# Performance work log

Measured on AMD Instinct MI355X. Metric: run time of the kernel, lower is better.

## Reference

```python
import jax, jax.numpy as jnp
import numpy as np

INPUT_SIZE = 1024
HIDDEN_SIZE = 1024
BATCH = 8192


def setup_inputs() -> dict:
    key = jax.random.key(0)
    ks = jax.random.split(key, 10)
    s_in = 1.0 / np.sqrt(INPUT_SIZE)
    s_h = 1.0 / np.sqrt(HIDDEN_SIZE)
    return {
        "input": jax.random.normal(ks[0], (BATCH, INPUT_SIZE), jnp.float32),
        "hx": jax.random.normal(ks[1], (BATCH, HIDDEN_SIZE), jnp.float32),
        # weights stored [in, out] (transpose of torch Linear)
        "W_ih": jax.random.uniform(ks[2], (INPUT_SIZE, 2 * HIDDEN_SIZE), jnp.float32, -s_in, s_in),
        "b_ih": jax.random.uniform(ks[3], (2 * HIDDEN_SIZE,), jnp.float32, -s_in, s_in),
        "W_hh": jax.random.uniform(ks[4], (HIDDEN_SIZE, 2 * HIDDEN_SIZE), jnp.float32, -s_h, s_h),
        "b_hh": jax.random.uniform(ks[5], (2 * HIDDEN_SIZE,), jnp.float32, -s_h, s_h),
        "W_c": jax.random.uniform(ks[6], (INPUT_SIZE, HIDDEN_SIZE), jnp.float32, -s_in, s_in),
        "b_c": jax.random.uniform(ks[7], (HIDDEN_SIZE,), jnp.float32, -s_in, s_in),
        "W_hc": jax.random.uniform(ks[8], (HIDDEN_SIZE, HIDDEN_SIZE), jnp.float32, -s_h, s_h),
        "b_hc": jax.random.uniform(ks[9], (HIDDEN_SIZE,), jnp.float32, -s_h, s_h),
    }


def reference(input, hx, W_ih, b_ih, W_hh, b_hh, W_c, b_c, W_hc, b_hc):
    H = hx.shape[1]
    gates = jax.nn.sigmoid(input @ W_ih + b_ih + hx @ W_hh + b_hh)  # [B, 2H]
    z_t, r_t = gates[:, :H], gates[:, H:]
    candidate = jnp.tanh(input @ W_c + b_c + r_t * (hx @ W_hc + b_hc))
    return (1.0 - z_t) * hx + z_t * candidate
```

## Files before the change

kernel.cpp:

```cpp
#include <hip/hip_runtime.h>
#include <hip/hip_bf16.h>
#include <cmath>


typedef __attribute__((ext_vector_type(8))) short bf16x8;
typedef __attribute__((ext_vector_type(4))) float f32x4;
typedef unsigned int u32;

typedef const __attribute__((address_space(1))) u32 gu32;
typedef __attribute__((address_space(3))) u32 su32;

__device__ __forceinline__ unsigned short f2bf(float f) {
  union { float f; u32 u; } v; v.f = f;
  u32 u = v.u;
  u += 0x7FFFu + ((u >> 16) & 1u);
  return (unsigned short)(u >> 16);
}

__device__ __forceinline__ void gload16(void* ldsp, const void* gp) {
  __builtin_amdgcn_global_load_lds((gu32*)gp, (su32*)ldsp, 16, 0, 0);
}

__device__ __forceinline__ float sigmf(float x) { return 1.0f / (1.0f + __expf(-x)); }

__global__ __launch_bounds__(256) void cvt_all(
    const float* __restrict__ In, const float* __restrict__ Hx,
    const float* __restrict__ Wih, const float* __restrict__ Whh,
    const float* __restrict__ Wc,  const float* __restrict__ Whc,
    unsigned short* __restrict__ wsIn, unsigned short* __restrict__ wsHx,
    unsigned short* __restrict__ wsWih, unsigned short* __restrict__ wsWhh,
    unsigned short* __restrict__ wsWc,  unsigned short* __restrict__ wsWhc)
{
  int bid = blockIdx.x;
  if (bid < 8192) {
    int gid = bid * 256 + threadIdx.x;
    const float* src; unsigned short* dst; int idx;
    if (gid < (1 << 20)) { src = In; dst = wsIn; idx = gid; }
    else                 { src = Hx; dst = wsHx; idx = gid - (1 << 20); }
    int m = idx >> 7;
    int t = idx & 127;
    const float4* s = (const float4*)(src + (size_t)m * 1024 + t * 8);
    float4 a = s[0], b = s[1];
    int row = m & 127;
    size_t tile = (size_t)(m >> 7) * 32 + (t >> 2);
    int sw = (t & 3) ^ ((row >> 1) & 3);
    bf16x8 v;
    v[0] = (short)f2bf(a.x); v[1] = (short)f2bf(a.y); v[2] = (short)f2bf(a.z); v[3] = (short)f2bf(a.w);
    v[4] = (short)f2bf(b.x); v[5] = (short)f2bf(b.y); v[6] = (short)f2bf(b.z); v[7] = (short)f2bf(b.w);
    *(bf16x8*)(dst + tile * 4096 + row * 32 + sw * 8) = v;
  } else {
    int wb = bid - 8192;
    const float* W; unsigned short* dst; int NW; int local;
    if (wb < 1024)      { W = Wih; dst = wsWih; NW = 2048; local = wb; }
    else if (wb < 2048) { W = Whh; dst = wsWhh; NW = 2048; local = wb - 1024; }
    else if (wb < 2560) { W = Wc;  dst = wsWc;  NW = 1024; local = wb - 2048; }
    else                { W = Whc; dst = wsWhc; NW = 1024; local = wb - 2560; }
    int nb = local >> 5, kb = local & 31;
    int n  = nb * 64 + (threadIdx.x & 63);
    int k0 = kb * 32 + (threadIdx.x >> 6) * 8;
    unsigned short h[8];
    #pragma unroll
    for (int b = 0; b < 8; ++b) h[b] = f2bf(W[(size_t)(k0 + b) * NW + n]);
    int row = n & 63;
    size_t tile = (size_t)(n >> 6) * 32 + (k0 >> 5);
    int sw = ((k0 >> 3) & 3) ^ ((row >> 1) & 3);
    bf16x8 v;
    #pragma unroll
    for (int b = 0; b < 8; ++b) v[b] = (short)h[b];
    *(bf16x8*)(dst + tile * 2048 + row * 32 + sw * 8) = v;
  }
}

__global__ __launch_bounds__(512, 2) void gru_gemm(
    const unsigned short* __restrict__ wsIn, const unsigned short* __restrict__ wsHx,
    const unsigned short* __restrict__ wsWih, const unsigned short* __restrict__ wsWhh,
    const unsigned short* __restrict__ wsWc, const unsigned short* __restrict__ wsWhc,
    const float* __restrict__ Hx,
    const float* __restrict__ bih, const float* __restrict__ bhh,
    const float* __restrict__ bc, const float* __restrict__ bhc,
    float* __restrict__ out)
{
  __shared__ unsigned short lds[57344];
  const int tid  = threadIdx.x;
  const int lane = tid & 63;
  const int wave = tid >> 6;
  const int wm = wave >> 1, wn = wave & 1;
  const int bid = blockIdx.x;
  const int swz = (bid & 7) * 64 + (bid >> 3);
  const int j = swz & 15;
  const int i = swz >> 4;

  const unsigned short* srcB[7];
  int strd[7];
  #pragma unroll
  for (int c0 = 0; c0 < 7; ++c0) {
    int c = wave * 7 + c0;
    const unsigned short* p; int st;
    if (c < 16) {
      int mt = 2 * i + (c >> 3);
      p = wsIn + (size_t)mt * 131072 + (c & 7) * 512; st = 4096;
    } else if (c < 32) {
      int cc = c - 16; int mt = 2 * i + (cc >> 3);
      p = wsHx + (size_t)mt * 131072 + (cc & 7) * 512; st = 4096;
    } else {
      int t = (c - 32) >> 2, cc = (c - 32) & 3;
      const unsigned short* base; int nb;
      if (t == 0)      { base = wsWih; nb = j; }
      else if (t == 1) { base = wsWih; nb = j + 16; }
      else if (t == 2) { base = wsWhh; nb = j; }
      else if (t == 3) { base = wsWhh; nb = j + 16; }
      else if (t == 4) { base = wsWc;  nb = j; }
      else             { base = wsWhc; nb = j; }
      p = base + (size_t)nb * 65536 + cc * 512; st = 2048;
    }
    srcB[c0] = p + lane * 8;
    strd[c0] = st;
  }
  const int ldsC = wave * 3584;

  f32x4 accZ[4][2], accR[4][2], accC[4][2], accH[4][2];
  #pragma unroll
  for (int a = 0; a < 4; ++a)
    #pragma unroll
    for (int b = 0; b < 2; ++b) {
      accZ[a][b] = (f32x4)(0.0f); accR[a][b] = (f32x4)(0.0f);
      accC[a][b] = (f32x4)(0.0f); accH[a][b] = (f32x4)(0.0f);
    }

  const int r15 = lane & 15;
  const int q   = lane >> 4;

  int aOff[4], wOff[2];
  #pragma unroll
  for (int mr = 0; mr < 4; ++mr) {
    int gr = wm * 64 + mr * 16 + r15;
    aOff[mr] = (gr >> 7) * 4096 + (gr & 127) * 32 + ((q ^ ((gr >> 1) & 3)) << 3);
  }
  #pragma unroll
  for (int nr = 0; nr < 2; ++nr) {
    int wr = wn * 32 + nr * 16 + r15;
    wOff[nr] = 16384 + wr * 32 + ((q ^ ((wr >> 1) & 3)) << 3);
  }

  auto stage = [&](int B, int s) {
    #pragma unroll
    for (int c0 = 0; c0 < 7; ++c0)
      gload16((void*)&lds[B + ldsC + c0 * 512],
              (const void*)(srcB[c0] + (size_t)s * strd[c0]));
  };

  auto step = [&](int B, int s2) {
    bf16x8 aIn[4], aHx[4];
    #pragma unroll
    for (int mr = 0; mr < 4; ++mr) {
      aIn[mr] = *(const bf16x8*)&lds[B + aOff[mr]];
      aHx[mr] = *(const bf16x8*)&lds[B + 8192 + aOff[mr]];
    }
    __builtin_amdgcn_s_setprio(1);
    {
      bf16x8 wa[2], wb[2];
      #pragma unroll
      for (int nr = 0; nr < 2; ++nr) {
        wa[nr] = *(const bf16x8*)&lds[B + wOff[nr]];
        wb[nr] = *(const bf16x8*)&lds[B + 4096 + wOff[nr]];
      }
      #pragma unroll
      for (int mr = 0; mr < 4; ++mr)
        #pragma unroll
        for (int nr = 0; nr < 2; ++nr) {
          accZ[mr][nr] = __builtin_amdgcn_mfma_f32_16x16x32_bf16(aIn[mr], wa[nr], accZ[mr][nr], 0, 0, 0);
          accZ[mr][nr] = __builtin_amdgcn_mfma_f32_16x16x32_bf16(aHx[mr], wb[nr], accZ[mr][nr], 0, 0, 0);
        }
    }
    {
      bf16x8 wa[2], wb[2];
      #pragma unroll
      for (int nr = 0; nr < 2; ++nr) {
        wa[nr] = *(const bf16x8*)&lds[B + 2048 + wOff[nr]];
        wb[nr] = *(const bf16x8*)&lds[B + 6144 + wOff[nr]];
      }
      #pragma unroll
      for (int mr = 0; mr < 4; ++mr)
        #pragma unroll
        for (int nr = 0; nr < 2; ++nr) {
          accR[mr][nr] = __builtin_amdgcn_mfma_f32_16x16x32_bf16(aIn[mr], wa[nr], accR[mr][nr], 0, 0, 0);
          accR[mr][nr] = __builtin_amdgcn_mfma_f32_16x16x32_bf16(aHx[mr], wb[nr], accR[mr][nr], 0, 0, 0);
        }
    }
    {
      bf16x8 wa[2], wb[2];
      #pragma unroll
      for (int nr = 0; nr < 2; ++nr) {
        wa[nr] = *(const bf16x8*)&lds[B + 8192 + wOff[nr]];
        wb[nr] = *(const bf16x8*)&lds[B + 10240 + wOff[nr]];
      }
      #pragma unroll
      for (int mr = 0; mr < 4; ++mr)
        #pragma unroll
        for (int nr = 0; nr < 2; ++nr) {
          accC[mr][nr] = __builtin_amdgcn_mfma_f32_16x16x32_bf16(aIn[mr], wa[nr], accC[mr][nr], 0, 0, 0);
          accH[mr][nr] = __builtin_amdgcn_mfma_f32_16x16x32_bf16(aHx[mr], wb[nr], accH[mr][nr], 0, 0, 0);
        }
    }
    __builtin_amdgcn_s_setprio(0);
    asm volatile("s_waitcnt lgkmcnt(0)" ::: "memory");
    __builtin_amdgcn_s_barrier();
    stage(B, s2);
    asm volatile("s_waitcnt vmcnt(7)" ::: "memory");
    __builtin_amdgcn_s_barrier();
  };

  stage(0, 0);
  stage(28672, 1);
  asm volatile("s_waitcnt vmcnt(7)" ::: "memory");
  __builtin_amdgcn_s_barrier();

  #pragma unroll 1
  for (int it = 0; it < 16; ++it) {
    const int s = it * 2;
    step(0,     s + 2 <= 31 ? s + 2 : 31);
    step(28672, s + 3 <= 31 ? s + 3 : 31);
  }

  const int n0 = j * 64 + wn * 32;
  const int m0 = i * 256 + wm * 64;
  #pragma unroll
  for (int nr = 0; nr < 2; ++nr) {
    int n = n0 + nr * 16 + r15;
    float bz  = bih[n] + bhh[n];
    float br  = bih[1024 + n] + bhh[1024 + n];
    float bcv = bc[n], bhcv = bhc[n];
    #pragma unroll
    for (int mr = 0; mr < 4; ++mr) {
      #pragma unroll
      for (int v = 0; v < 4; ++v) {
        int m = m0 + mr * 16 + q * 4 + v;
        float z  = sigmf(accZ[mr][nr][v] + bz);
        float rr = sigmf(accR[mr][nr][v] + br);
        float cd = tanhf(accC[mr][nr][v] + bcv + rr * (accH[mr][nr][v] + bhcv));
        float h  = Hx[(size_t)m * 1024 + n];
        out[(size_t)m * 1024 + n] = (1.0f - z) * h + z * cd;
      }
    }
  }
}

__global__ __launch_bounds__(256) void gru_fallback(
    const float* __restrict__ In, const float* __restrict__ Hx,
    const float* __restrict__ Wih, const float* __restrict__ bih,
    const float* __restrict__ Whh, const float* __restrict__ bhh,
    const float* __restrict__ Wc, const float* __restrict__ bc,
    const float* __restrict__ Whc, const float* __restrict__ bhc,
    float* __restrict__ out)
{
  __shared__ float sIn[64][17], sHx[64][17];
  __shared__ float sW[6][16][68];
  const int tid = threadIdx.x;
  const int j = blockIdx.x & 15, i = blockIdx.x >> 4;
  const int tx = tid & 15, ty = tid >> 4;
  float accZ[4][4] = {}, accR[4][4] = {}, accC[4][4] = {}, accH[4][4] = {};
  const int ms = tid >> 2, kq = (tid & 3) * 4;
  const int wk = tid >> 4, wn4 = (tid & 15) * 4;
  for (int k0 = 0; k0 < 1024; k0 += 16) {
    __syncthreads();
    {
      float4 a = *(const float4*)&In[(size_t)(i * 64 + ms) * 1024 + k0 + kq];
      sIn[ms][kq] = a.x; sIn[ms][kq + 1] = a.y; sIn[ms][kq + 2] = a.z; sIn[ms][kq + 3] = a.w;
      float4 b = *(const float4*)&Hx[(size_t)(i * 64 + ms) * 1024 + k0 + kq];
      sHx[ms][kq] = b.x; sHx[ms][kq + 1] = b.y; sHx[ms][kq + 2] = b.z; sHx[ms][kq + 3] = b.w;
    }
    {
      float4 w0 = *(const float4*)&Wih[(size_t)(k0 + wk) * 2048 + j * 64 + wn4];
      float4 w1 = *(const float4*)&Wih[(size_t)(k0 + wk) * 2048 + 1024 + j * 64 + wn4];
      float4 w2 = *(const float4*)&Whh[(size_t)(k0 + wk) * 2048 + j * 64 + wn4];
      float4 w3 = *(const float4*)&Whh[(size_t)(k0 + wk) * 2048 + 1024 + j * 64 + wn4];
      float4 w4 = *(const float4*)&Wc[(size_t)(k0 + wk) * 1024 + j * 64 + wn4];
      float4 w5 = *(const float4*)&Whc[(size_t)(k0 + wk) * 1024 + j * 64 + wn4];
      sW[0][wk][wn4] = w0.x; sW[0][wk][wn4+1] = w0.y; sW[0][wk][wn4+2] = w0.z; sW[0][wk][wn4+3] = w0.w;
      sW[1][wk][wn4] = w1.x; sW[1][wk][wn4+1] = w1.y; sW[1][wk][wn4+2] = w1.z; sW[1][wk][wn4+3] = w1.w;
      sW[2][wk][wn4] = w2.x; sW[2][wk][wn4+1] = w2.y; sW[2][wk][wn4+2] = w2.z; sW[2][wk][wn4+3] = w2.w;
      sW[3][wk][wn4] = w3.x; sW[3][wk][wn4+1] = w3.y; sW[3][wk][wn4+2] = w3.z; sW[3][wk][wn4+3] = w3.w;
      sW[4][wk][wn4] = w4.x; sW[4][wk][wn4+1] = w4.y; sW[4][wk][wn4+2] = w4.z; sW[4][wk][wn4+3] = w4.w;
      sW[5][wk][wn4] = w5.x; sW[5][wk][wn4+1] = w5.y; sW[5][wk][wn4+2] = w5.z; sW[5][wk][wn4+3] = w5.w;
    }
    __syncthreads();
    for (int kk = 0; kk < 16; ++kk) {
      float aI[4], aH[4];
      #pragma unroll
      for (int im = 0; im < 4; ++im) { aI[im] = sIn[ty * 4 + im][kk]; aH[im] = sHx[ty * 4 + im][kk]; }
      #pragma unroll
      for (int jn = 0; jn < 4; ++jn) {
        float w0 = sW[0][kk][tx * 4 + jn], w1 = sW[1][kk][tx * 4 + jn], w2 = sW[2][kk][tx * 4 + jn];
        float w3 = sW[3][kk][tx * 4 + jn], w4 = sW[4][kk][tx * 4 + jn], w5 = sW[5][kk][tx * 4 + jn];
        #pragma unroll
        for (int im = 0; im < 4; ++im) {
          accZ[im][jn] += aI[im] * w0 + aH[im] * w2;
          accR[im][jn] += aI[im] * w1 + aH[im] * w3;
          accC[im][jn] += aI[im] * w4;
          accH[im][jn] += aH[im] * w5;
        }
      }
    }
  }
  #pragma unroll
  for (int jn = 0; jn < 4; ++jn) {
    int n = j * 64 + tx * 4 + jn;
    float bz  = bih[n] + bhh[n];
    float br  = bih[1024 + n] + bhh[1024 + n];
    float bcv = bc[n], bhcv = bhc[n];
    #pragma unroll
    for (int im = 0; im < 4; ++im) {
      int m = i * 64 + ty * 4 + im;
      float z  = sigmf(accZ[im][jn] + bz);
      float rr = sigmf(accR[im][jn] + br);
      float cd = tanhf(accC[im][jn] + bcv + rr * (accH[im][jn] + bhcv));
      float h  = Hx[(size_t)m * 1024 + n];
      out[(size_t)m * 1024 + n] = (1.0f - z) * h + z * cd;
    }
  }
}

extern "C" void kernel_launch(void* const* d_in, const int* in_sizes, int n_in,
                              void* d_out, int out_size, void* d_ws, size_t ws_size,
                              hipStream_t stream) {
  const float* In  = (const float*)d_in[0];
  const float* Hx  = (const float*)d_in[1];
  const float* Wih = (const float*)d_in[2];
  const float* bih = (const float*)d_in[3];
  const float* Whh = (const float*)d_in[4];
  const float* bhh = (const float*)d_in[5];
  const float* Wc  = (const float*)d_in[6];
  const float* bc  = (const float*)d_in[7];
  const float* Whc = (const float*)d_in[8];
  const float* bhc = (const float*)d_in[9];
  float* out = (float*)d_out;

  const size_t WS_NEED = 46137344ull;
  if (ws_size >= WS_NEED) {
    unsigned short* ws    = (unsigned short*)d_ws;
    unsigned short* wsIn  = ws;
    unsigned short* wsHx  = ws + 8388608;
    unsigned short* wsWih = ws + 16777216;
    unsigned short* wsWhh = ws + 18874368;
    unsigned short* wsWc  = ws + 20971520;
    unsigned short* wsWhc = ws + 22020096;
    cvt_all<<<11264, 256, 0, stream>>>(In, Hx, Wih, Whh, Wc, Whc,
                                       wsIn, wsHx, wsWih, wsWhh, wsWc, wsWhc);
    gru_gemm<<<512, 512, 0, stream>>>(wsIn, wsHx, wsWih, wsWhh, wsWc, wsWhc,
                                      Hx, bih, bhh, bc, bhc, out);
  } else {
    gru_fallback<<<2048, 256, 0, stream>>>(In, Hx, Wih, bih, Whh, bhh, Wc, bc, Whc, bhc, out);
  }
}
```

Before: 135.6 us.

## Interleave global-to-LDS staging between MFMA phases within each k-step

Restructures the main GEMM loop so the next-stage global_load_lds copies are issued piecewise between the Z, R and C/H MFMA phases instead of all after compute. The LDS layout is reordered so the weight chunks consumed first are loaded earliest, with one chunk (Wc/Whc) prefetched into the other buffer a step ahead. The aim is to overlap memory traffic with tensor-core work, at the cost of more barriers per step and a more fragile wait-count scheme.

```diff
diff --git a/kernel.cpp b/kernel.cpp
--- a/kernel.cpp
+++ b/kernel.cpp
@@ -16,12 +16,14 @@
   u += 0x7FFFu + ((u >> 16) & 1u);
   return (unsigned short)(u >> 16);
 }
-
 __device__ __forceinline__ void gload16(void* ldsp, const void* gp) {
   __builtin_amdgcn_global_load_lds((gu32*)gp, (su32*)ldsp, 16, 0, 0);
 }
-
 __device__ __forceinline__ float sigmf(float x) { return 1.0f / (1.0f + __expf(-x)); }
+
+#define LGKM0 do { asm volatile("s_waitcnt lgkmcnt(0)" ::: "memory"); __builtin_amdgcn_sched_barrier(0); } while (0)
+#define VMC6  do { asm volatile("s_waitcnt vmcnt(6)"   ::: "memory"); __builtin_amdgcn_sched_barrier(0); } while (0)
+#define BARR  __builtin_amdgcn_s_barrier()
 
 __global__ __launch_bounds__(256) void cvt_all(
     const float* __restrict__ In, const float* __restrict__ Hx,
@@ -37,8 +39,7 @@
     const float* src; unsigned short* dst; int idx;
     if (gid < (1 << 20)) { src = In; dst = wsIn; idx = gid; }
     else                 { src = Hx; dst = wsHx; idx = gid - (1 << 20); }
-    int m = idx >> 7;
-    int t = idx & 127;
+    int m = idx >> 7, t = idx & 127;
     const float4* s = (const float4*)(src + (size_t)m * 1024 + t * 8);
     float4 a = s[0], b = s[1];
     int row = m & 127;
@@ -58,15 +59,12 @@
     int nb = local >> 5, kb = local & 31;
     int n  = nb * 64 + (threadIdx.x & 63);
     int k0 = kb * 32 + (threadIdx.x >> 6) * 8;
-    unsigned short h[8];
-    #pragma unroll
-    for (int b = 0; b < 8; ++b) h[b] = f2bf(W[(size_t)(k0 + b) * NW + n]);
+    bf16x8 v;
+    #pragma unroll
+    for (int b = 0; b < 8; ++b) v[b] = (short)f2bf(W[(size_t)(k0 + b) * NW + n]);
     int row = n & 63;
     size_t tile = (size_t)(n >> 6) * 32 + (k0 >> 5);
     int sw = ((k0 >> 3) & 3) ^ ((row >> 1) & 3);
-    bf16x8 v;
-    #pragma unroll
-    for (int b = 0; b < 8; ++b) v[b] = (short)h[b];
     *(bf16x8*)(dst + tile * 2048 + row * 32 + sw * 8) = v;
   }
 }
@@ -89,34 +87,27 @@
   const int swz = (bid & 7) * 64 + (bid >> 3);
   const int j = swz & 15;
   const int i = swz >> 4;
-
-  const unsigned short* srcB[7];
-  int strd[7];
-  #pragma unroll
-  for (int c0 = 0; c0 < 7; ++c0) {
-    int c = wave * 7 + c0;
-    const unsigned short* p; int st;
-    if (c < 16) {
-      int mt = 2 * i + (c >> 3);
-      p = wsIn + (size_t)mt * 131072 + (c & 7) * 512; st = 4096;
-    } else if (c < 32) {
-      int cc = c - 16; int mt = 2 * i + (cc >> 3);
-      p = wsHx + (size_t)mt * 131072 + (cc & 7) * 512; st = 4096;
-    } else {
-      int t = (c - 32) >> 2, cc = (c - 32) & 3;
-      const unsigned short* base; int nb;
-      if (t == 0)      { base = wsWih; nb = j; }
-      else if (t == 1) { base = wsWih; nb = j + 16; }
-      else if (t == 2) { base = wsWhh; nb = j; }
-      else if (t == 3) { base = wsWhh; nb = j + 16; }
-      else if (t == 4) { base = wsWc;  nb = j; }
-      else             { base = wsWhc; nb = j; }
-      p = base + (size_t)nb * 65536 + cc * 512; st = 2048;
-    }
-    srcB[c0] = p + lane * 8;
-    strd[c0] = st;
-  }
-  const int ldsC = wave * 3584;
+  const int r15 = lane & 15, q = lane >> 4;
+
+  auto chunkSrc = [&](int c, const unsigned short*& p, int& st) {
+    if (c < 16)      { p = wsIn + (size_t)(2 * i + (c >> 3)) * 131072 + (c & 7) * 512; st = 4096; }
+    else if (c < 32) { int cc = c - 16; p = wsHx + (size_t)(2 * i + (cc >> 3)) * 131072 + (cc & 7) * 512; st = 4096; }
+    else if (c < 36) { p = wsWih + (size_t)j * 65536        + (c - 32) * 512; st = 2048; }
+    else if (c < 40) { p = wsWhh + (size_t)j * 65536        + (c - 36) * 512; st = 2048; }
+    else if (c < 44) { p = wsWih + (size_t)(j + 16) * 65536 + (c - 40) * 512; st = 2048; }
+    else if (c < 48) { p = wsWhh + (size_t)(j + 16) * 65536 + (c - 44) * 512; st = 2048; }
+    else if (c < 52) { p = wsWc  + (size_t)j * 65536        + (c - 48) * 512; st = 2048; }
+    else             { p = wsWhc + (size_t)j * 65536        + (c - 52) * 512; st = 2048; }
+    p += lane * 8;
+  };
+  const unsigned short* p2[5]; int s2[5];
+  #pragma unroll
+  for (int k = 0; k < 5; ++k) chunkSrc(wave * 5 + k, p2[k], s2[k]);
+  const unsigned short* p3; int s3; chunkSrc(40 + wave, p3, s3);
+  const unsigned short* p1; int s1; chunkSrc(48 + wave, p1, s1);
+  const int d2 = wave * 5 * 512;
+  const int d3 = (40 + wave) * 512;
+  const int d1 = (48 + wave) * 512;
 
   f32x4 accZ[4][2], accR[4][2], accC[4][2], accH[4][2];
   #pragma unroll
@@ -127,9 +118,6 @@
       accC[a][b] = (f32x4)(0.0f); accH[a][b] = (f32x4)(0.0f);
     }
 
-  const int r15 = lane & 15;
-  const int q   = lane >> 4;
-
   int aOff[4], wOff[2];
   #pragma unroll
   for (int mr = 0; mr < 4; ++mr) {
@@ -139,88 +127,87 @@
   #pragma unroll
   for (int nr = 0; nr < 2; ++nr) {
     int wr = wn * 32 + nr * 16 + r15;
-    wOff[nr] = 16384 + wr * 32 + ((q ^ ((wr >> 1) & 3)) << 3);
-  }
-
-  auto stage = [&](int B, int s) {
-    #pragma unroll
-    for (int c0 = 0; c0 < 7; ++c0)
-      gload16((void*)&lds[B + ldsC + c0 * 512],
-              (const void*)(srcB[c0] + (size_t)s * strd[c0]));
-  };
-
-  auto step = [&](int B, int s2) {
-    bf16x8 aIn[4], aHx[4];
+    wOff[nr] = wr * 32 + ((q ^ ((wr >> 1) & 3)) << 3);
+  }
+
+  #define MFMA16(AI, AH, WA, WB, ACC)                                                \
+    __builtin_amdgcn_s_setprio(1);                                                   \
+    _Pragma("unroll")                                                                \
+    for (int mr_ = 0; mr_ < 4; ++mr_)                                                \
+      _Pragma("unroll")                                                              \
+      for (int nr_ = 0; nr_ < 2; ++nr_) {                                            \
+        ACC[mr_][nr_] = __builtin_amdgcn_mfma_f32_16x16x32_bf16(AI[mr_], WA[nr_], ACC[mr_][nr_], 0, 0, 0); \
+        ACC[mr_][nr_] = __builtin_amdgcn_mfma_f32_16x16x32_bf16(AH[mr_], WB[nr_], ACC[mr_][nr_], 0, 0, 0); \
+      }                                                                              \
+    __builtin_amdgcn_s_setprio(0);
+
+  auto step = [&](int B, int OB, int sP1, int sP23) {
+    bf16x8 aIn[4], aHx[4], wA[2], wB[2];
     #pragma unroll
     for (int mr = 0; mr < 4; ++mr) {
       aIn[mr] = *(const bf16x8*)&lds[B + aOff[mr]];
       aHx[mr] = *(const bf16x8*)&lds[B + 8192 + aOff[mr]];
     }
+    #pragma unroll
+    for (int nr = 0; nr < 2; ++nr) {
+      wA[nr] = *(const bf16x8*)&lds[B + 16384 + wOff[nr]];
+      wB[nr] = *(const bf16x8*)&lds[B + 18432 + wOff[nr]];
+    }
+    gload16((void*)&lds[OB + d1], (const void*)(p1 + (size_t)sP1 * s1));
+    BARR;
+    LGKM0;
+    MFMA16(aIn, aHx, wA, wB, accZ)
+    BARR;
+    #pragma unroll
+    for (int nr = 0; nr < 2; ++nr) {
+      wA[nr] = *(const bf16x8*)&lds[B + 20480 + wOff[nr]];
+      wB[nr] = *(const bf16x8*)&lds[B + 22528 + wOff[nr]];
+    }
+    #pragma unroll
+    for (int k = 0; k < 5; ++k)
+      gload16((void*)&lds[B + d2 + k * 512], (const void*)(p2[k] + (size_t)sP23 * s2[k]));
+    BARR;
+    LGKM0;
+    MFMA16(aIn, aHx, wA, wB, accR)
+    BARR;
+    #pragma unroll
+    for (int nr = 0; nr < 2; ++nr) {
+      wA[nr] = *(const bf16x8*)&lds[B + 24576 + wOff[nr]];
+      wB[nr] = *(const bf16x8*)&lds[B + 26624 + wOff[nr]];
+    }
+    gload16((void*)&lds[B + d3], (const void*)(p3 + (size_t)sP23 * s3));
+    BARR;
+    LGKM0;
     __builtin_amdgcn_s_setprio(1);
-    {
-      bf16x8 wa[2], wb[2];
+    #pragma unroll
+    for (int mr_ = 0; mr_ < 4; ++mr_)
       #pragma unroll
-      for (int nr = 0; nr < 2; ++nr) {
-        wa[nr] = *(const bf16x8*)&lds[B + wOff[nr]];
-        wb[nr] = *(const bf16x8*)&lds[B + 4096 + wOff[nr]];
+      for (int nr_ = 0; nr_ < 2; ++nr_) {
+        accC[mr_][nr_] = __builtin_amdgcn_mfma_f32_16x16x32_bf16(aIn[mr_], wA[nr_], accC[mr_][nr_], 0, 0, 0);
+        accH[mr_][nr_] = __builtin_amdgcn_mfma_f32_16x16x32_bf16(aHx[mr_], wB[nr_], accH[mr_][nr_], 0, 0, 0);
       }
-      #pragma unroll
-      for (int mr = 0; mr < 4; ++mr)
-        #pragma unroll
-        for (int nr = 0; nr < 2; ++nr) {
-          accZ[mr][nr] = __builtin_amdgcn_mfma_f32_16x16x32_bf16(aIn[mr], wa[nr], accZ[mr][nr], 0, 0, 0);
-          accZ[mr][nr] = __builtin_amdgcn_mfma_f32_16x16x32_bf16(aHx[mr], wb[nr], accZ[mr][nr], 0, 0, 0);
-        }
-    }
-    {
-      bf16x8 wa[2], wb[2];
-      #pragma unroll
-      for (int nr = 0; nr < 2; ++nr) {
-        wa[nr] = *(const bf16x8*)&lds[B + 2048 + wOff[nr]];
-        wb[nr] = *(const bf16x8*)&lds[B + 6144 + wOff[nr]];
-      }
-      #pragma unroll
-      for (int mr = 0; mr < 4; ++mr)
-        #pragma unroll
-        for (int nr = 0; nr < 2; ++nr) {
-          accR[mr][nr] = __builtin_amdgcn_mfma_f32_16x16x32_bf16(aIn[mr], wa[nr], accR[mr][nr], 0, 0, 0);
-          accR[mr][nr] = __builtin_amdgcn_mfma_f32_16x16x32_bf16(aHx[mr], wb[nr], accR[mr][nr], 0, 0, 0);
-        }
-    }
-    {
-      bf16x8 wa[2], wb[2];
-      #pragma unroll
-      for (int nr = 0; nr < 2; ++nr) {
-        wa[nr] = *(const bf16x8*)&lds[B + 8192 + wOff[nr]];
-        wb[nr] = *(const bf16x8*)&lds[B + 10240 + wOff[nr]];
-      }
-      #pragma unroll
-      for (int mr = 0; mr < 4; ++mr)
-        #pragma unroll
-        for (int nr = 0; nr < 2; ++nr) {
-          accC[mr][nr] = __builtin_amdgcn_mfma_f32_16x16x32_bf16(aIn[mr], wa[nr], accC[mr][nr], 0, 0, 0);
-          accH[mr][nr] = __builtin_amdgcn_mfma_f32_16x16x32_bf16(aHx[mr], wb[nr], accH[mr][nr], 0, 0, 0);
-        }
-    }
     __builtin_amdgcn_s_setprio(0);
-    asm volatile("s_waitcnt lgkmcnt(0)" ::: "memory");
-    __builtin_amdgcn_s_barrier();
-    stage(B, s2);
-    asm volatile("s_waitcnt vmcnt(7)" ::: "memory");
-    __builtin_amdgcn_s_barrier();
+    VMC6;
+    BARR;
   };
 
-  stage(0, 0);
-  stage(28672, 1);
-  asm volatile("s_waitcnt vmcnt(7)" ::: "memory");
-  __builtin_amdgcn_s_barrier();
+  #pragma unroll
+  for (int k = 0; k < 5; ++k) gload16((void*)&lds[d2 + k * 512], (const void*)p2[k]);
+  gload16((void*)&lds[d3], (const void*)p3);
+  gload16((void*)&lds[d1], (const void*)p1);
+  #pragma unroll
+  for (int k = 0; k < 5; ++k) gload16((void*)&lds[28672 + d2 + k * 512], (const void*)(p2[k] + s2[k]));
+  gload16((void*)&lds[28672 + d3], (const void*)(p3 + s3));
+  VMC6;
+  BARR;
 
   #pragma unroll 1
   for (int it = 0; it < 16; ++it) {
-    const int s = it * 2;
-    step(0,     s + 2 <= 31 ? s + 2 : 31);
-    step(28672, s + 3 <= 31 ? s + 3 : 31);
-  }
+    const int s = 2 * it;
+    step(0,     28672, s + 1 <= 31 ? s + 1 : 31, s + 2 <= 31 ? s + 2 : 31);
+    step(28672, 0,     s + 2 <= 31 ? s + 2 : 31, s + 3 <= 31 ? s + 3 : 31);
+  }
+  #undef MFMA16
 
   const int n0 = j * 64 + wn * 32;
   const int m0 = i * 256 + wm * 64;
```

New measurement: 133.4 us. No clear change (-1.7%).
